# Performance work log

Measured on AMD Instinct MI355X. Metric: run time of the kernel, lower is better.

The kernel has to match this reference:

```python
import jax, jax.numpy as jnp
import numpy as np

N_OUT = 4096
N_IN = 4096
FRAC_SPARSE = 0.5
N_SPARSE = int(FRAC_SPARSE * N_OUT * N_IN)  # 8388608
TOKENS = 256


def setup_inputs() -> dict:
    key = jax.random.key(0)
    k1, k2 = jax.random.split(key)
    # x: activations fed to F.linear
    x = jax.random.normal(k1, (TOKENS, N_IN), dtype=jnp.float32)
    # sparse_values: nn.Parameter of size n_sparse
    sparse_values = jax.random.normal(k2, (N_SPARSE,), dtype=jnp.float32) * 0.02
    # sparse_mask as sorted unique row-major flat indices of True entries.
    # torch `out[mask] = values` fills values into True positions in row-major
    # order, which equals scattering values at the ascending-sorted flat idxs.
    rng = np.random.default_rng(0)
    flat_idx = np.sort(rng.permutation(N_OUT * N_IN)[:N_SPARSE]).astype(np.int32)
    return {"x": x, "sparse_values": sparse_values, "flat_idx": jnp.asarray(flat_idx)}


def reference(x, sparse_values, flat_idx):
    # reconstruct(): dense [n_out, n_in] weight via scatter of sparse values
    W = (
        jnp.zeros((N_OUT * N_IN,), dtype=sparse_values.dtype)
        .at[flat_idx]
        .set(sparse_values)
        .reshape(N_OUT, N_IN)
    )
    # F.linear(x, W) == x @ W.T
    return x @ W.T
```

## Files before the change

kernel.cpp:

```cpp
#include <hip/hip_runtime.h>
#include <stdint.h>

#define N_OUT    4096
#define N_IN     4096
#define TOKENS   256
#define N_SPARSE 8388608
#define SPLITK   16
#define KCHUNK   (N_IN / SPLITK)
#define BN       64
#define BK       64
#define CPW      (SPLITK + 1)

typedef __attribute__((ext_vector_type(8))) short bf16x8;
typedef __attribute__((ext_vector_type(8))) unsigned short u16x8;
typedef __attribute__((ext_vector_type(4))) float f32x4;

__device__ __forceinline__ unsigned short f2bf(float f) {
    union { float f; unsigned u; } v; v.f = f;
    unsigned r = v.u + 0x7fffu + ((v.u >> 16) & 1u);
    return (unsigned short)(r >> 16);
}

__device__ __forceinline__ float bf2f(unsigned short u) {
    union { unsigned u; float f; } v; v.u = ((unsigned)u) << 16;
    return v.f;
}

__device__ __forceinline__ void gload_lds16(const void* g, void* l) {
    __builtin_amdgcn_global_load_lds(
        (const __attribute__((address_space(1))) void*)g,
        (__attribute__((address_space(3))) void*)l, 16, 0, 0);
}

__global__ void convert_x(const float* __restrict__ x, unsigned short* __restrict__ xb) {
    int i = (blockIdx.x * 256 + threadIdx.x) * 4;
    const float4 v = *(const float4*)(x + i);
    ushort4 o;
    o.x = f2bf(v.x); o.y = f2bf(v.y); o.z = f2bf(v.z); o.w = f2bf(v.w);
    *(ushort4*)(xb + i) = o;
}

__global__ void col_ptr_k(const int* __restrict__ idx, int* __restrict__ cp) {
    const int e = blockIdx.x * 256 + threadIdx.x;
    if (e >= N_OUT * CPW) return;
    const int r = e / CPW;
    const int z = e - r * CPW;
    const int target = r * N_IN + z * KCHUNK;
    int lo = 0, hi = N_SPARSE;
    while (lo < hi) { int m = (lo + hi) >> 1; if (idx[m] < target) lo = m + 1; else hi = m; }
    cp[e] = lo;
}

__global__ __launch_bounds__(512) void fused_gemm(
        const unsigned short* __restrict__ xb,
        const int* __restrict__ idx,
        const float* __restrict__ vals,
        const int* __restrict__ cp,
        unsigned short* __restrict__ part)
{
    __shared__ short As[TOKENS * BK];
    __shared__ short Bs[BN * KCHUNK];

    const int tid = threadIdx.x;
    const int l   = tid & 63;
    const int w   = tid >> 6;
    const int bn  = blockIdx.x;
    const int bz  = blockIdx.y;

    {
        const u16x8 z8 = {};
        unsigned short* b0 = (unsigned short*)Bs + tid * 32;
        *(u16x8*)(b0)      = z8; *(u16x8*)(b0 + 8)  = z8;
        *(u16x8*)(b0 + 16) = z8; *(u16x8*)(b0 + 24) = z8;
    }
    __syncthreads();

    const int srow8 = l >> 3;
    const int sgq   = (l & 7) ^ srow8;
    const int kbase = bz * KCHUNK;
    #pragma unroll
    for (int io = 0; io < 4; ++io) {
        const int rbase = io * 64 + w * 8;
        gload_lds16(xb + (size_t)(rbase + srow8) * N_IN + kbase + sgq * 8,
                    &As[rbase * BK]);
    }

    {
        const int rl   = tid >> 3;
        const int sub  = tid & 7;
        const int r    = bn * BN + rl;
        const int base = r * N_IN + kbase;
        const int start = cp[r * CPW + bz];
        const int end   = cp[r * CPW + bz + 1];
        unsigned short* brow = (unsigned short*)Bs + rl * KCHUNK;
        const int rx = (rl & 7) << 3;
        for (int j = start + sub; j < end; j += 8) {
            const int c = idx[j] - base;
            brow[((c & ~7) ^ rx) | (c & 7)] = f2bf(vals[j]);
        }
    }
    __syncthreads();

    const int wm  = w >> 1;
    const int wn  = w & 1;
    const int lr  = l & 15;
    const int lkg = l >> 4;
    f32x4 acc[4][2] = {};

    for (int t = 0; t < KCHUNK / BK; ++t) {
        #pragma unroll
        for (int kk = 0; kk < 2; ++kk) {
            const int ksl = kk * 4 + lkg;
            bf16x8 af[4], bfr[2];
            #pragma unroll
            for (int i = 0; i < 4; ++i) {
                const int m = wm * 64 + i * 16 + lr;
                af[i] = *(const bf16x8*)&As[m * BK + ((ksl ^ (m & 7)) << 3)];
            }
            #pragma unroll
            for (int i = 0; i < 2; ++i) {
                const int n   = wn * 32 + i * 16 + lr;
                const int gsl = t * 8 + ksl;
                bfr[i] = *(const bf16x8*)&Bs[n * KCHUNK + ((gsl ^ (n & 7)) << 3)];
            }
            #pragma unroll
            for (int mi = 0; mi < 4; ++mi)
                #pragma unroll
                for (int ni = 0; ni < 2; ++ni)
                    acc[mi][ni] = __builtin_amdgcn_mfma_f32_16x16x32_bf16(
                                      af[mi], bfr[ni], acc[mi][ni], 0, 0, 0);
        }
        __syncthreads();
        if (t + 1 < KCHUNK / BK) {
            #pragma unroll
            for (int io = 0; io < 4; ++io) {
                const int rbase = io * 64 + w * 8;
                gload_lds16(xb + (size_t)(rbase + srow8) * N_IN + kbase + (t + 1) * BK + sgq * 8,
                            &As[rbase * BK]);
            }
            __syncthreads();
        }
    }

    unsigned short* po = part + (size_t)bz * (TOKENS * N_OUT) + (size_t)bn * BN;
    #pragma unroll
    for (int mi = 0; mi < 4; ++mi)
        #pragma unroll
        for (int r = 0; r < 4; ++r) {
            const int m = wm * 64 + mi * 16 + lkg * 4 + r;
            #pragma unroll
            for (int ni = 0; ni < 2; ++ni) {
                const int n = wn * 32 + ni * 16 + lr;
                po[(size_t)m * N_OUT + n] = f2bf(acc[mi][ni][r]);
            }
        }
}

__global__ void reduce_k(const unsigned short* __restrict__ part, float* __restrict__ out) {
    const int i = (blockIdx.x * 256 + threadIdx.x) * 8;
    float a[8] = {};
    for (int z = 0; z < SPLITK; ++z) {
        const u16x8 p = *(const u16x8*)(part + (size_t)z * (TOKENS * N_OUT) + i);
        #pragma unroll
        for (int j = 0; j < 8; ++j) a[j] += bf2f((unsigned short)p[j]);
    }
    float4 o0 = { a[0], a[1], a[2], a[3] };
    float4 o1 = { a[4], a[5], a[6], a[7] };
    *(float4*)(out + i)     = o0;
    *(float4*)(out + i + 4) = o1;
}

__global__ void fallback_rowcsr(const float* __restrict__ x, const float* __restrict__ vals,
                                const int* __restrict__ idx, float* __restrict__ out) {
    const int o = blockIdx.x;
    const int t = threadIdx.x;
    __shared__ int   scol[256];
    __shared__ float sval[256];

    int lo = 0, hi = N_SPARSE;
    const int target = o * N_IN;
    while (lo < hi) { int m = (lo + hi) >> 1; if (idx[m] < target) lo = m + 1; else hi = m; }
    const int start = lo;
    hi = N_SPARSE;
    const int target2 = target + N_IN;
    while (lo < hi) { int m = (lo + hi) >> 1; if (idx[m] < target2) lo = m + 1; else hi = m; }
    const int end = lo;

    float acc = 0.f;
    const float* xr = x + (size_t)t * N_IN;
    for (int base = start; base < end; base += 256) {
        const int k = base + t;
        if (k < end) { scol[t] = idx[k] - target; sval[t] = vals[k]; }
        __syncthreads();
        const int cnt = min(256, end - base);
        for (int j = 0; j < cnt; ++j) acc += sval[j] * xr[scol[j]];
        __syncthreads();
    }
    out[(size_t)t * N_OUT + o] = acc;
}

extern "C" void kernel_launch(void* const* d_in, const int* in_sizes, int n_in,
                              void* d_out, int out_size, void* d_ws, size_t ws_size,
                              hipStream_t stream) {
    const float* x    = (const float*)d_in[0];
    const float* vals = (const float*)d_in[1];
    const int*   idx  = (const int*)d_in[2];
    float* out = (float*)d_out;

    const size_t part_bytes = (size_t)SPLITK * TOKENS * N_OUT * 2;
    const size_t xb_bytes   = (size_t)TOKENS * N_IN * 2;
    const size_t cp_bytes   = (size_t)N_OUT * CPW * 4;
    const size_t need = part_bytes + xb_bytes + cp_bytes;

    if (ws_size >= need) {
        unsigned short* part = (unsigned short*)d_ws;
        unsigned short* xb   = (unsigned short*)((char*)d_ws + part_bytes);
        int*            cp   = (int*)((char*)d_ws + part_bytes + xb_bytes);

        convert_x<<<(TOKENS * N_IN) / 1024, 256, 0, stream>>>(x, xb);
        col_ptr_k<<<(N_OUT * CPW + 255) / 256, 256, 0, stream>>>(idx, cp);
        dim3 grid(N_OUT / BN, SPLITK);
        fused_gemm<<<grid, 512, 0, stream>>>(xb, idx, vals, cp, part);
        reduce_k<<<(TOKENS * N_OUT) / 2048, 256, 0, stream>>>(part, out);
    } else {
        fallback_rowcsr<<<N_OUT, TOKENS, 0, stream>>>(x, vals, idx, out);
    }
}
```

Measured before the change: 56.09 us.

## Halve split-K, load A directly from global, vectorize sparse scatter, merge prep kernels

Merges the x conversion and column-pointer search into one launch. Halves split-K to 8, so each block now processes two 256-wide K chunks in turn, rebuilding the B tile in shared memory for each. A fragments are now read straight from global memory instead of being staged through LDS with async loads, and the sparse index/value scatter uses int4/float4 loads with bounds masks. This aims to cut launch overhead, the number of partial-sum buffers written and reduced, and scatter load instructions. The cost is uncoalesced, unshared global reads of A in the MMA loop and less grid parallelism.

Measured after the change: 65.41 us, median of 5. 1.17x slower.

```diff
diff --git a/kernel.cpp b/kernel.cpp
--- a/kernel.cpp
+++ b/kernel.cpp
@@ -5,11 +5,12 @@
 #define N_IN     4096
 #define TOKENS   256
 #define N_SPARSE 8388608
-#define SPLITK   16
-#define KCHUNK   (N_IN / SPLITK)
+#define SPLITK   8
+#define KCHUNK   256
+#define NCHUNK   2
+#define NSEG     (N_IN / KCHUNK)
+#define CPW      (NSEG + 1)
 #define BN       64
-#define BK       64
-#define CPW      (SPLITK + 1)
 
 typedef __attribute__((ext_vector_type(8))) short bf16x8;
 typedef __attribute__((ext_vector_type(8))) unsigned short u16x8;
@@ -26,29 +27,25 @@
     return v.f;
 }
 
-__device__ __forceinline__ void gload_lds16(const void* g, void* l) {
-    __builtin_amdgcn_global_load_lds(
-        (const __attribute__((address_space(1))) void*)g,
-        (__attribute__((address_space(3))) void*)l, 16, 0, 0);
-}
-
-__global__ void convert_x(const float* __restrict__ x, unsigned short* __restrict__ xb) {
-    int i = (blockIdx.x * 256 + threadIdx.x) * 4;
-    const float4 v = *(const float4*)(x + i);
-    ushort4 o;
-    o.x = f2bf(v.x); o.y = f2bf(v.y); o.z = f2bf(v.z); o.w = f2bf(v.w);
-    *(ushort4*)(xb + i) = o;
-}
-
-__global__ void col_ptr_k(const int* __restrict__ idx, int* __restrict__ cp) {
-    const int e = blockIdx.x * 256 + threadIdx.x;
-    if (e >= N_OUT * CPW) return;
-    const int r = e / CPW;
-    const int z = e - r * CPW;
-    const int target = r * N_IN + z * KCHUNK;
-    int lo = 0, hi = N_SPARSE;
-    while (lo < hi) { int m = (lo + hi) >> 1; if (idx[m] < target) lo = m + 1; else hi = m; }
-    cp[e] = lo;
+__global__ void prep(const float* __restrict__ x, const int* __restrict__ idx,
+                     unsigned short* __restrict__ xb, int* __restrict__ cp) {
+    const int b = blockIdx.x;
+    const int t = threadIdx.x;
+    if (b < 1024) {
+        const int i = (b * 256 + t) * 4;
+        const float4 v = *(const float4*)(x + i);
+        ushort4 o;
+        o.x = f2bf(v.x); o.y = f2bf(v.y); o.z = f2bf(v.z); o.w = f2bf(v.w);
+        *(ushort4*)(xb + i) = o;
+    } else {
+        const int e = (b - 1024) * 256 + t;
+        const int r = e / CPW;
+        const int z = e - r * CPW;
+        const int target = r * N_IN + z * KCHUNK;
+        int lo = 0, hi = N_SPARSE;
+        while (lo < hi) { int m = (lo + hi) >> 1; if (idx[m] < target) lo = m + 1; else hi = m; }
+        cp[e] = lo;
+    }
 }
 
 __global__ __launch_bounds__(512) void fused_gemm(
@@ -58,7 +55,6 @@
         const int* __restrict__ cp,
         unsigned short* __restrict__ part)
 {
-    __shared__ short As[TOKENS * BK];
     __shared__ short Bs[BN * KCHUNK];
 
     const int tid = threadIdx.x;
@@ -67,61 +63,64 @@
     const int bn  = blockIdx.x;
     const int bz  = blockIdx.y;
 
-    {
-        const u16x8 z8 = {};
-        unsigned short* b0 = (unsigned short*)Bs + tid * 32;
-        *(u16x8*)(b0)      = z8; *(u16x8*)(b0 + 8)  = z8;
-        *(u16x8*)(b0 + 16) = z8; *(u16x8*)(b0 + 24) = z8;
-    }
-    __syncthreads();
-
-    const int srow8 = l >> 3;
-    const int sgq   = (l & 7) ^ srow8;
-    const int kbase = bz * KCHUNK;
-    #pragma unroll
-    for (int io = 0; io < 4; ++io) {
-        const int rbase = io * 64 + w * 8;
-        gload_lds16(xb + (size_t)(rbase + srow8) * N_IN + kbase + sgq * 8,
-                    &As[rbase * BK]);
-    }
-
-    {
-        const int rl   = tid >> 3;
-        const int sub  = tid & 7;
-        const int r    = bn * BN + rl;
-        const int base = r * N_IN + kbase;
-        const int start = cp[r * CPW + bz];
-        const int end   = cp[r * CPW + bz + 1];
-        unsigned short* brow = (unsigned short*)Bs + rl * KCHUNK;
-        const int rx = (rl & 7) << 3;
-        for (int j = start + sub; j < end; j += 8) {
-            const int c = idx[j] - base;
-            brow[((c & ~7) ^ rx) | (c & 7)] = f2bf(vals[j]);
-        }
-    }
-    __syncthreads();
-
     const int wm  = w >> 1;
     const int wn  = w & 1;
     const int lr  = l & 15;
     const int lkg = l >> 4;
+    const int kbase0 = bz * (KCHUNK * NCHUNK);
+
+    const int rl   = tid >> 3;
+    const int sub  = tid & 7;
+    const int rx   = (rl & 7) << 3;
+    unsigned short* brow = (unsigned short*)Bs + rl * KCHUNK;
+    const int rglob = bn * BN + rl;
+
     f32x4 acc[4][2] = {};
 
-    for (int t = 0; t < KCHUNK / BK; ++t) {
-        #pragma unroll
-        for (int kk = 0; kk < 2; ++kk) {
-            const int ksl = kk * 4 + lkg;
+    for (int c = 0; c < NCHUNK; ++c) {
+        {
+            const u16x8 z8 = {};
+            unsigned short* b0 = (unsigned short*)Bs + tid * 32;
+            *(u16x8*)(b0)      = z8; *(u16x8*)(b0 + 8)  = z8;
+            *(u16x8*)(b0 + 16) = z8; *(u16x8*)(b0 + 24) = z8;
+        }
+        __syncthreads();
+
+        {
+            const int seg   = bz * NCHUNK + c;
+            const int start = cp[rglob * CPW + seg];
+            const int end   = cp[rglob * CPW + seg + 1];
+            const int base  = rglob * N_IN + kbase0 + c * KCHUNK;
+            for (int jb = (start & ~3) + sub * 4; jb < end; jb += 32) {
+                const int4   i4 = *(const int4*)(idx + jb);
+                const float4 v4 = *(const float4*)(vals + jb);
+                #pragma unroll
+                for (int e = 0; e < 4; ++e) {
+                    const int j  = jb + e;
+                    const int ic = (&i4.x)[e];
+                    if (j >= start && j < end) {
+                        const int cc = ic - base;
+                        brow[((cc & ~7) ^ rx) | (cc & 7)] = f2bf((&v4.x)[e]);
+                    }
+                }
+            }
+        }
+        __syncthreads();
+
+        const unsigned short* ap = xb + kbase0 + c * KCHUNK + lkg * 8;
+        #pragma unroll 2
+        for (int kk = 0; kk < KCHUNK / 32; ++kk) {
             bf16x8 af[4], bfr[2];
             #pragma unroll
             for (int i = 0; i < 4; ++i) {
                 const int m = wm * 64 + i * 16 + lr;
-                af[i] = *(const bf16x8*)&As[m * BK + ((ksl ^ (m & 7)) << 3)];
+                af[i] = *(const bf16x8*)(ap + (size_t)m * N_IN + kk * 32);
             }
             #pragma unroll
             for (int i = 0; i < 2; ++i) {
-                const int n   = wn * 32 + i * 16 + lr;
-                const int gsl = t * 8 + ksl;
-                bfr[i] = *(const bf16x8*)&Bs[n * KCHUNK + ((gsl ^ (n & 7)) << 3)];
+                const int n    = wn * 32 + i * 16 + lr;
+                const int slot = (kk * 4 + lkg) ^ (n & 7);
+                bfr[i] = *(const bf16x8*)&Bs[n * KCHUNK + slot * 8];
             }
             #pragma unroll
             for (int mi = 0; mi < 4; ++mi)
@@ -131,15 +130,6 @@
                                       af[mi], bfr[ni], acc[mi][ni], 0, 0, 0);
         }
         __syncthreads();
-        if (t + 1 < KCHUNK / BK) {
-            #pragma unroll
-            for (int io = 0; io < 4; ++io) {
-                const int rbase = io * 64 + w * 8;
-                gload_lds16(xb + (size_t)(rbase + srow8) * N_IN + kbase + (t + 1) * BK + sgq * 8,
-                            &As[rbase * BK]);
-            }
-            __syncthreads();
-        }
     }
 
     unsigned short* po = part + (size_t)bz * (TOKENS * N_OUT) + (size_t)bn * BN;
@@ -217,8 +207,7 @@
         unsigned short* xb   = (unsigned short*)((char*)d_ws + part_bytes);
         int*            cp   = (int*)((char*)d_ws + part_bytes + xb_bytes);
 
-        convert_x<<<(TOKENS * N_IN) / 1024, 256, 0, stream>>>(x, xb);
-        col_ptr_k<<<(N_OUT * CPW + 255) / 256, 256, 0, stream>>>(idx, cp);
+        prep<<<1024 + (N_OUT * CPW) / 256, 256, 0, stream>>>(x, idx, xb, cp);
         dim3 grid(N_OUT / BN, SPLITK);
         fused_gemm<<<grid, 512, 0, stream>>>(xb, idx, vals, cp, part);
         reduce_k<<<(TOKENS * N_OUT) / 2048, 256, 0, stream>>>(part, out);
```
